# Performance work log

Measured on AMD Instinct MI355X. Metric: run time of the kernel, lower is better.

The kernel has to match this reference:

```python
import jax, jax.numpy as jnp
import numpy as np

B, H, W, C = 4, 112, 112, 256
WS, E, HEADS = 7, 3, 8
HD = C // HEADS                      # 32
WA = WS * WS                         # 49
NWIN = (H // WS) * (W // WS)         # 256
FOCAL_AREA = 49                      # focal_window^2
SCALE = HD ** -0.5

def _valid_ind_rolled():
    tl = np.ones((WS, WS)); tl[:-E, :-E] = 0
    tr = np.ones((WS, WS)); tr[:-E, E:] = 0
    bl = np.ones((WS, WS)); bl[E:, :-E] = 0
    br = np.ones((WS, WS)); br[E:, E:] = 0
    msk = np.stack([tl, tr, bl, br], 0).reshape(-1)
    return np.nonzero(msk == 1)[0]

VALID_IND = jnp.asarray(_valid_ind_rolled())   # (132,)
L_ROLL = WA + int(VALID_IND.shape[0])          # 181 = window_size_of_key

def window_partition(t):
    b = t.shape[0]
    t = t.reshape(b, H // WS, WS, W // WS, WS, C)
    return t.transpose(0, 1, 3, 2, 4, 5).reshape(-1, WA, C)

def split_heads(t):  # (n, L, C) -> (n, HEADS, L, HD)
    n, L, _ = t.shape
    return t.reshape(n, L, HEADS, HD).transpose(0, 2, 1, 3)

def setup_inputs():
    key = jax.random.key(0)
    ks = jax.random.split(key, 9)
    p = lambda k, s: jax.random.normal(k, s, jnp.float32) * 0.02
    return {
        "x": jax.random.normal(ks[0], (B, H, W, C), jnp.float32),
        "x_expanded": jax.random.normal(ks[1], (B * NWIN, 4 * WA, C), jnp.float32),
        "x_pooled": jax.random.normal(ks[2], (B * NWIN, FOCAL_AREA, C), jnp.float32),
        "mask_pooled": jnp.zeros((1, NWIN, FOCAL_AREA), jnp.float32),
        "q_w": p(ks[3], (C, C)), "q_b": jnp.zeros((C,), jnp.float32),
        "k_w": p(ks[4], (C, C)), "k_b": jnp.zeros((C,), jnp.float32),
        "v_w": p(ks[5], (C, C)), "v_b": jnp.zeros((C,), jnp.float32),
        "proj_w": p(ks[6], (C, C)), "proj_b": jnp.zeros((C,), jnp.float32),
        "rpb": p(ks[7], (1, HEADS, WA, L_ROLL)),
        "rpb_pooled": p(ks[8], (HEADS, WA, FOCAL_AREA)),
    }

def reference(x, x_expanded, x_pooled, mask_pooled,
              q_w, q_b, k_w, k_b, v_w, v_b, proj_w, proj_b,
              rpb, rpb_pooled):
    lin = lambda t, w, b: t @ w.T + b
    # window-local q/k/v: (B*NWIN, HEADS, WA, HD)
    q = split_heads(window_partition(lin(x, q_w, q_b))) * SCALE
    k_win = split_heads(window_partition(lin(x, k_w, k_b)))
    v_win = split_heads(window_partition(lin(x, v_w, v_b)))
    # expanded (rolled) keys/values, gathered by static valid indices
    xe = x_expanded[:, VALID_IND]                       # (B*NWIN, 132, C)
    k_exp = split_heads(lin(xe, k_w, k_b))
    v_exp = split_heads(lin(xe, v_w, v_b))
    # focal-pooled keys/values
    k_pool = split_heads(lin(x_pooled, k_w, k_b))
    v_pool = split_heads(lin(x_pooled, v_w, v_b))

    k_all = jnp.concatenate([k_win, k_exp, k_pool], axis=2)  # (B*NWIN,h,N,hd)
    v_all = jnp.concatenate([v_win, v_exp, v_pool], axis=2)

    attn = jnp.einsum("whqd,whkd->whqk", q, k_all)            # (B*NWIN,h,WA,N)
    attn = attn.at[:, :, :, :L_ROLL].add(rpb)
    mask_b = jnp.broadcast_to(
        mask_pooled[:, :, None, None, :], (B, NWIN, 1, 1, FOCAL_AREA)
    ).reshape(-1, 1, 1, FOCAL_AREA)
    attn = attn.at[:, :, :, L_ROLL:].add(rpb_pooled[None] + mask_b)
    attn = jax.nn.softmax(attn, axis=-1)
    out = jnp.einsum("whqk,whkd->whqd", attn, v_all)          # (B*NWIN,h,WA,hd)
    out = out.transpose(0, 2, 1, 3).reshape(-1, WA, C)
    return lin(out, proj_w, proj_b)
```

## Files before the change

### kernel.cpp

```cpp
#include <hip/hip_runtime.h>

typedef __attribute__((ext_vector_type(8))) __bf16 bf16x8;
typedef __attribute__((ext_vector_type(4))) float f32x4;

#define SCALE_Q 0.17677669529663687f

__constant__ int VALID_IND_C[132] = {
  4,5,6, 11,12,13, 18,19,20, 25,26,27,
  28,29,30,31,32,33,34, 35,36,37,38,39,40,41, 42,43,44,45,46,47,48,
  49,50,51, 56,57,58, 63,64,65, 70,71,72,
  77,78,79,80,81,82,83, 84,85,86,87,88,89,90, 91,92,93,94,95,96,97,
  98,99,100,101,102,103,104, 105,106,107,108,109,110,111, 112,113,114,115,116,117,118,
  123,124,125, 130,131,132, 137,138,139, 144,145,146,
  147,148,149,150,151,152,153, 154,155,156,157,158,159,160, 161,162,163,164,165,166,167,
  168,169,170, 175,176,177, 182,183,184, 189,190,191
};

__device__ __forceinline__ unsigned short f2bf(float f) {
  unsigned int u = __float_as_uint(f);
  u += 0x7fffu + ((u >> 16) & 1u);
  return (unsigned short)(u >> 16);
}

__device__ __forceinline__ uint4 pack8(const float4 a, const float4 b) {
  uint4 r;
  r.x = (unsigned)f2bf(a.x) | ((unsigned)f2bf(a.y) << 16);
  r.y = (unsigned)f2bf(a.z) | ((unsigned)f2bf(a.w) << 16);
  r.z = (unsigned)f2bf(b.x) | ((unsigned)f2bf(b.y) << 16);
  r.w = (unsigned)f2bf(b.z) | ((unsigned)f2bf(b.w) << 16);
  return r;
}

__global__ void prep_weights(const float* __restrict__ qw, const float* __restrict__ kw,
                             const float* __restrict__ vw, const float* __restrict__ pw,
                             unsigned short* __restrict__ wp) {
  int gid = blockIdx.x * 256 + threadIdx.x;
  int wsel = gid >> 16;
  int d = gid & 65535;
  const float* W = wsel == 0 ? qw : wsel == 1 ? kw : wsel == 2 ? vw : pw;
  int e = d & 7, ln = (d >> 3) & 63, ks = (d >> 9) & 7, cf = d >> 12;
  int c = cf * 16 + (ln & 15);
  int k = ks * 32 + ((ln >> 4) << 3) + e;
  wp[gid] = f2bf(W[c * 256 + k]);
}

__global__ void prep_bias(const float* __restrict__ rpb, const float* __restrict__ rpbp,
                          float* __restrict__ biasp) {
  int idx = blockIdx.x * 256 + threadIdx.x;
  int q = idx & 63, key = (idx >> 6) & 255, h = idx >> 14;
  int qc = q < 49 ? q : 48;
  float v;
  if (key < 181)      v = rpb[(h * 49 + qc) * 181 + key];
  else if (key < 230) v = rpbp[(h * 49 + qc) * 49 + (key - 181)];
  else                v = -1e30f;
  biasp[idx] = v;
}

__device__ __forceinline__ const float* kv_src_row(int w, int l, const float* x,
                                                   const float* xe, const float* xp) {
  if (l >= 230) l = 229;
  if (l < 49) {
    int b = w >> 8, win = w & 255;
    int wy = win >> 4, wx = win & 15;
    int iy = l / 7, ix = l - iy * 7;
    return x + (((b * 112 + wy * 7 + iy) * 112) + wx * 7 + ix) * 256;
  } else if (l < 181) {
    return xe + (w * 196 + VALID_IND_C[l - 49]) * 256;
  } else {
    return xp + (w * 49 + (l - 181)) * 256;
  }
}

__device__ __forceinline__ void gemm_core(const char* smem, const unsigned short* Wp,
                                          int nfbase, int lane, f32x4 acc[4][4]) {
  int arow = lane & 15, ahi = lane >> 4;
#pragma unroll
  for (int ks = 0; ks < 8; ++ks) {
    bf16x8 a[4];
#pragma unroll
    for (int m = 0; m < 4; ++m)
      a[m] = *(const bf16x8*)(smem + (m * 16 + arow) * 528 + ks * 64 + ahi * 16);
#pragma unroll
    for (int n = 0; n < 4; ++n) {
      bf16x8 b = *(const bf16x8*)(Wp + (((nfbase + n) * 8 + ks) * 64 + lane) * 8);
#pragma unroll
      for (int m = 0; m < 4; ++m)
        acc[m][n] = __builtin_amdgcn_mfma_f32_16x16x32_bf16(a[m], b, acc[m][n], 0, 0, 0);
    }
  }
}

__global__ __launch_bounds__(512, 4) void kv_gemm(
    const float* __restrict__ x, const float* __restrict__ xe, const float* __restrict__ xp,
    const float* __restrict__ kb, const float* __restrict__ vb,
    const unsigned short* __restrict__ WpK, const unsigned short* __restrict__ WpV,
    unsigned short* __restrict__ Kg, unsigned short* __restrict__ Vtg) {
  __shared__ char smem[64 * 528];
  __shared__ char tbuf[256 * 144];
  int tid = threadIdx.x;
  int w = blockIdx.x >> 2, sub = blockIdx.x & 3;
  {
    int r = tid >> 3, seg = tid & 7;
    const float* src = kv_src_row(w, sub * 64 + r, x, xe, xp) + seg * 32;
    char* dst = smem + r * 528 + seg * 64;
#pragma unroll
    for (int i = 0; i < 4; ++i) {
      float4 a = ((const float4*)src)[i * 2];
      float4 b = ((const float4*)src)[i * 2 + 1];
      *(uint4*)(dst + i * 16) = pack8(a, b);
    }
  }
  __syncthreads();
  int lane = tid & 63, wv = tid >> 6;
  bool isV = wv >= 4;
  int colq = wv & 3;
  const unsigned short* Wp = isV ? WpV : WpK;
  f32x4 acc[4][4];
#pragma unroll
  for (int m = 0; m < 4; ++m)
#pragma unroll
    for (int n = 0; n < 4; ++n) acc[m][n] = (f32x4){0.f, 0.f, 0.f, 0.f};
  gemm_core(smem, Wp, colq * 4, lane, acc);

  int arow = lane & 15, ahi = lane >> 4;
  const float* bias = isV ? vb : kb;
  __syncthreads();
  if (!isV) {
#pragma unroll
    for (int n = 0; n < 4; ++n) {
      int c = colq * 64 + n * 16 + arow;
      float bc = bias[c];
#pragma unroll
      for (int m = 0; m < 4; ++m)
#pragma unroll
        for (int reg = 0; reg < 4; ++reg)
          *(unsigned short*)(smem + (m * 16 + ahi * 4 + reg) * 528 + c * 2) =
              f2bf(acc[m][n][reg] + bc);
    }
  } else {
#pragma unroll
    for (int n = 0; n < 4; ++n) {
      int c = colq * 64 + n * 16 + arow;
      float bc = bias[c];
#pragma unroll
      for (int m = 0; m < 4; ++m)
#pragma unroll
        for (int reg = 0; reg < 4; ++reg)
          *(unsigned short*)(tbuf + c * 144 + (m * 16 + ahi * 4 + reg) * 2) =
              f2bf(acc[m][n][reg] + bc);
    }
  }
  __syncthreads();
  {
    int r = tid >> 3, seg = tid & 7;
    unsigned short* dst = Kg + (unsigned)(w * 256 + sub * 64 + r) * 256 + seg * 32;
    const char* s = smem + r * 528 + seg * 64;
#pragma unroll
    for (int i = 0; i < 4; ++i) *(uint4*)(dst + i * 8) = *(const uint4*)(s + i * 16);
  }
  {
    int c = tid >> 1, hf = tid & 1;
    unsigned short* dst = Vtg + (unsigned)(w * 256 + c) * 256 + sub * 64 + hf * 32;
    const char* s = tbuf + c * 144 + hf * 64;
#pragma unroll
    for (int i = 0; i < 4; ++i) *(uint4*)(dst + i * 8) = *(const uint4*)(s + i * 16);
  }
}

__global__ __launch_bounds__(256, 4) void q_gemm(
    const float* __restrict__ x, const float* __restrict__ qb,
    const unsigned short* __restrict__ WpQ, unsigned short* __restrict__ Qg) {
  __shared__ char smem[64 * 528];
  int tid = threadIdx.x;
  int w = blockIdx.x;
  int b = w >> 8, win = w & 255, wy = win >> 4, wx = win & 15;
  {
    int r = tid >> 2, seg = tid & 3;
    int rr = r < 49 ? r : 48;
    int iy = rr / 7, ix = rr - iy * 7;
    const float* src = x + (((b * 112 + wy * 7 + iy) * 112) + wx * 7 + ix) * 256 + seg * 64;
    char* dst = smem + r * 528 + seg * 128;
#pragma unroll
    for (int i = 0; i < 8; ++i) {
      float4 a = ((const float4*)src)[i * 2];
      float4 bb = ((const float4*)src)[i * 2 + 1];
      *(uint4*)(dst + i * 16) = pack8(a, bb);
    }
  }
  __syncthreads();
  int lane = tid & 63, wv = tid >> 6;
  f32x4 acc[4][4];
#pragma unroll
  for (int m = 0; m < 4; ++m)
#pragma unroll
    for (int n = 0; n < 4; ++n) acc[m][n] = (f32x4){0.f, 0.f, 0.f, 0.f};
  gemm_core(smem, WpQ, wv * 4, lane, acc);

  int arow = lane & 15, ahi = lane >> 4;
  __syncthreads();
#pragma unroll
  for (int n = 0; n < 4; ++n) {
    int c = wv * 64 + n * 16 + arow;
    float bc = qb[c];
#pragma unroll
    for (int m = 0; m < 4; ++m)
#pragma unroll
      for (int reg = 0; reg < 4; ++reg)
        *(unsigned short*)(smem + (m * 16 + ahi * 4 + reg) * 528 + c * 2) =
            f2bf((acc[m][n][reg] + bc) * SCALE_Q);
  }
  __syncthreads();
  {
    int r = tid >> 2, seg = tid & 3;
    unsigned short* dst = Qg + (unsigned)(w * 64 + r) * 256 + seg * 64;
    const char* s = smem + r * 528 + seg * 128;
#pragma unroll
    for (int i = 0; i < 8; ++i) *(uint4*)(dst + i * 8) = *(const uint4*)(s + i * 16);
  }
}

__global__ __launch_bounds__(512, 2) void attn_kernel(
    const unsigned short* __restrict__ Qg, const unsigned short* __restrict__ Kg,
    const unsigned short* __restrict__ Vtg, const float* __restrict__ biasp,
    const float* __restrict__ maskp, unsigned short* __restrict__ Og) {
  __shared__ char sK[64 * 528];
  __shared__ char sV[256 * 144];
  __shared__ char sP[8 * 64 * 144];
  int tid = threadIdx.x, lane = tid & 63, h = tid >> 6;
  int w = blockIdx.x, win = w & 255;
  int arow = lane & 15, ahi = lane >> 4;

  bf16x8 qa[4];
#pragma unroll
  for (int m = 0; m < 4; ++m)
    qa[m] = *(const bf16x8*)(Qg + (unsigned)(w * 64 + m * 16 + arow) * 256 + h * 32 + ahi * 8);

  f32x4 o[4][2];
  float mrun[4][4], lrun[4][4];
#pragma unroll
  for (int m = 0; m < 4; ++m) {
#pragma unroll
    for (int r = 0; r < 4; ++r) { mrun[m][r] = -1e30f; lrun[m][r] = 0.f; }
    o[m][0] = (f32x4){0.f, 0.f, 0.f, 0.f};
    o[m][1] = (f32x4){0.f, 0.f, 0.f, 0.f};
  }
  char* myP = sP + h * 9216;

  for (int t = 0; t < 4; ++t) {
    int kb = t * 64;
    __syncthreads();
    {
      int r = tid >> 3, seg = tid & 7;
      const unsigned short* src = Kg + (unsigned)(w * 256 + kb + r) * 256 + seg * 32;
      char* dst = sK + r * 528 + seg * 64;
#pragma unroll
      for (int i = 0; i < 4; ++i) *(uint4*)(dst + i * 16) = *(const uint4*)(src + i * 8);
      int c = tid >> 1, hf = tid & 1;
      const unsigned short* vs = Vtg + (unsigned)(w * 256 + c) * 256 + kb + hf * 32;
      char* vd = sV + c * 144 + hf * 64;
#pragma unroll
      for (int i = 0; i < 4; ++i) *(uint4*)(vd + i * 16) = *(const uint4*)(vs + i * 8);
    }
    __syncthreads();

    f32x4 s[4][4];
    {
      bf16x8 kf[4];
#pragma unroll
      for (int n = 0; n < 4; ++n)
        kf[n] = *(const bf16x8*)(sK + (n * 16 + arow) * 528 + h * 64 + ahi * 16);
#pragma unroll
      for (int m = 0; m < 4; ++m)
#pragma unroll
        for (int n = 0; n < 4; ++n)
          s[m][n] = __builtin_amdgcn_mfma_f32_16x16x32_bf16(qa[m], kf[n],
                      (f32x4){0.f, 0.f, 0.f, 0.f}, 0, 0, 0);
    }
#pragma unroll
    for (int n = 0; n < 4; ++n) {
      int key = kb + n * 16 + arow;
      float mk = 0.f;
      if (key >= 181 && key < 230) mk = maskp[win * 49 + (key - 181)];
      bool kvalid = key < 230;
#pragma unroll
      for (int m = 0; m < 4; ++m) {
        f32x4 bfr = *(const f32x4*)(biasp + (h * 256 + key) * 64 + m * 16 + ahi * 4);
#pragma unroll
        for (int reg = 0; reg < 4; ++reg)
          s[m][n][reg] = kvalid ? (s[m][n][reg] + bfr[reg] + mk) : -1e30f;
      }
    }
#pragma unroll
    for (int m = 0; m < 4; ++m) {
#pragma unroll
      for (int reg = 0; reg < 4; ++reg) {
        float mx = fmaxf(fmaxf(s[m][0][reg], s[m][1][reg]), fmaxf(s[m][2][reg], s[m][3][reg]));
#pragma unroll
        for (int d = 1; d < 16; d <<= 1) mx = fmaxf(mx, __shfl_xor(mx, d));
        float mold = mrun[m][reg];
        float mnew = fmaxf(mold, mx);
        float sc = __expf(mold - mnew);
        float rs = 0.f;
#pragma unroll
        for (int n = 0; n < 4; ++n) {
          float p = __expf(s[m][n][reg] - mnew);
          s[m][n][reg] = p;
          rs += p;
        }
#pragma unroll
        for (int d = 1; d < 16; d <<= 1) rs += __shfl_xor(rs, d);
        lrun[m][reg] = lrun[m][reg] * sc + rs;
        mrun[m][reg] = mnew;
        o[m][0][reg] *= sc;
        o[m][1][reg] *= sc;
      }
    }
#pragma unroll
    for (int m = 0; m < 4; ++m)
#pragma unroll
      for (int n = 0; n < 4; ++n) {
        char* base = myP + (m * 16 + ahi * 4) * 144 + (n * 16 + arow) * 2;
#pragma unroll
        for (int reg = 0; reg < 4; ++reg)
          *(unsigned short*)(base + reg * 144) = f2bf(s[m][n][reg]);
      }
    bf16x8 vf[2][2];
#pragma unroll
    for (int n2 = 0; n2 < 2; ++n2)
#pragma unroll
      for (int kv = 0; kv < 2; ++kv)
        vf[n2][kv] = *(const bf16x8*)(sV + (h * 32 + n2 * 16 + arow) * 144 + kv * 64 + ahi * 16);
#pragma unroll
    for (int m = 0; m < 4; ++m)
#pragma unroll
      for (int kv = 0; kv < 2; ++kv) {
        bf16x8 pf = *(const bf16x8*)(myP + (m * 16 + arow) * 144 + kv * 64 + ahi * 16);
#pragma unroll
        for (int n2 = 0; n2 < 2; ++n2)
          o[m][n2] = __builtin_amdgcn_mfma_f32_16x16x32_bf16(pf, vf[n2][kv], o[m][n2], 0, 0, 0);
      }
  }
  __syncthreads();
#pragma unroll
  for (int m = 0; m < 4; ++m)
#pragma unroll
    for (int n2 = 0; n2 < 2; ++n2)
#pragma unroll
      for (int reg = 0; reg < 4; ++reg) {
        int qrow = m * 16 + ahi * 4 + reg;
        float val = o[m][n2][reg] / lrun[m][reg];
        *(unsigned short*)(sK + qrow * 528 + (h * 32 + n2 * 16 + arow) * 2) = f2bf(val);
      }
  __syncthreads();
  for (int i = tid; i < 49 * 32; i += 512) {
    int r = i >> 5, seg = i & 31;
    *(uint4*)(Og + (unsigned)(w * 49 + r) * 256 + seg * 8) = *(const uint4*)(sK + r * 528 + seg * 16);
  }
}

__global__ __launch_bounds__(256, 4) void proj_gemm(
    const unsigned short* __restrict__ Og, const float* __restrict__ pb,
    const unsigned short* __restrict__ WpP, float* __restrict__ out) {
  __shared__ char smem[64 * 528];
  int tid = threadIdx.x;
  {
    int r = tid >> 2, seg = tid & 3;
    const unsigned short* src = Og + (unsigned)(blockIdx.x * 64 + r) * 256 + seg * 64;
    char* dst = smem + r * 528 + seg * 128;
#pragma unroll
    for (int i = 0; i < 8; ++i)
      *(uint4*)(dst + i * 16) = *(const uint4*)(src + i * 8);
  }
  __syncthreads();
  int lane = tid & 63, wv = tid >> 6;
  f32x4 acc[4][4];
#pragma unroll
  for (int m = 0; m < 4; ++m)
#pragma unroll
    for (int n = 0; n < 4; ++n) acc[m][n] = (f32x4){0.f, 0.f, 0.f, 0.f};
  gemm_core(smem, WpP, wv * 4, lane, acc);

  int arow = lane & 15, ahi = lane >> 4;
#pragma unroll
  for (int n = 0; n < 4; ++n) {
    int c = wv * 64 + n * 16 + arow;
    float bc = pb[c];
#pragma unroll
    for (int m = 0; m < 4; ++m) {
      int g = blockIdx.x * 64 + m * 16 + ahi * 4;
#pragma unroll
      for (int reg = 0; reg < 4; ++reg)
        out[(unsigned)(g + reg) * 256 + c] = acc[m][n][reg] + bc;
    }
  }
}

extern "C" void kernel_launch(void* const* d_in, const int* in_sizes, int n_in,
                              void* d_out, int out_size, void* d_ws, size_t ws_size,
                              hipStream_t stream) {
  (void)in_sizes; (void)n_in; (void)out_size;
  const float* x    = (const float*)d_in[0];
  const float* xe   = (const float*)d_in[1];
  const float* xp   = (const float*)d_in[2];
  const float* mask = (const float*)d_in[3];
  const float* qw   = (const float*)d_in[4];
  const float* qb   = (const float*)d_in[5];
  const float* kw   = (const float*)d_in[6];
  const float* kb   = (const float*)d_in[7];
  const float* vw   = (const float*)d_in[8];
  const float* vb   = (const float*)d_in[9];
  const float* pw   = (const float*)d_in[10];
  const float* pb   = (const float*)d_in[11];
  const float* rpb  = (const float*)d_in[12];
  const float* rpbp = (const float*)d_in[13];

  char* ws = (char*)d_ws;
  if (ws_size < 328728576ull) return;
  unsigned short* Wp  = (unsigned short*)(ws);
  float* biasp        = (float*)(ws + 524288);
  unsigned short* Qg  = (unsigned short*)(ws + 1048576);
  unsigned short* Kg  = (unsigned short*)(ws + 1048576 + 33554432);
  unsigned short* Vtg = (unsigned short*)(ws + 1048576 + 33554432 + 134217728);
  unsigned short* Og  = (unsigned short*)(ws + 1048576 + 33554432 + 2 * 134217728);
  const unsigned short* WpQ = Wp;
  const unsigned short* WpK = Wp + 65536;
  const unsigned short* WpV = Wp + 131072;
  const unsigned short* WpP = Wp + 196608;

  hipLaunchKernelGGL(prep_weights, dim3(1024), dim3(256), 0, stream, qw, kw, vw, pw, Wp);
  hipLaunchKernelGGL(prep_bias,    dim3(512),  dim3(256), 0, stream, rpb, rpbp, biasp);
  hipLaunchKernelGGL(q_gemm,       dim3(1024), dim3(256), 0, stream, x, qb, WpQ, Qg);
  hipLaunchKernelGGL(kv_gemm,      dim3(4096), dim3(512), 0, stream,
                     x, xe, xp, kb, vb, WpK, WpV, Kg, Vtg);
  hipLaunchKernelGGL(attn_kernel,  dim3(1024), dim3(512), 0, stream,
                     Qg, Kg, Vtg, biasp, mask, Og);
  hipLaunchKernelGGL(proj_gemm,    dim3(784),  dim3(256), 0, stream, Og, pb, WpP, (float*)d_out);
}
```

Measured before the change: 745.0 us.

## Keep attention probabilities in registers and drop online softmax in attn kernel

Attention now computes transposed score tiles so the bf16 probability fragment feeds the PV MFMA straight from registers, loading K/V fragments directly from global memory instead of staging them in LDS with per-tile barriers. The online max/rescale softmax is replaced with an unnormalized exp and a final row-sum division, and the bias table is transposed to match. kv_gemm reuses one LDS buffer and skips writing padded key rows, and attn occupancy bound is raised. Dropping max subtraction risks overflow for large scores, and unwritten padded K rows rely on the -inf bias.

```diff
diff --git a/kernel.cpp b/kernel.cpp
--- a/kernel.cpp
+++ b/kernel.cpp
@@ -47,7 +47,7 @@
 __global__ void prep_bias(const float* __restrict__ rpb, const float* __restrict__ rpbp,
                           float* __restrict__ biasp) {
   int idx = blockIdx.x * 256 + threadIdx.x;
-  int q = idx & 63, key = (idx >> 6) & 255, h = idx >> 14;
+  int key = idx & 255, q = (idx >> 8) & 63, h = idx >> 14;
   int qc = q < 49 ? q : 48;
   float v;
   if (key < 181)      v = rpb[(h * 49 + qc) * 181 + key];
@@ -95,8 +95,7 @@
     const float* __restrict__ kb, const float* __restrict__ vb,
     const unsigned short* __restrict__ WpK, const unsigned short* __restrict__ WpV,
     unsigned short* __restrict__ Kg, unsigned short* __restrict__ Vtg) {
-  __shared__ char smem[64 * 528];
-  __shared__ char tbuf[256 * 144];
+  __shared__ char smem[256 * 144];
   int tid = threadIdx.x;
   int w = blockIdx.x >> 2, sub = blockIdx.x & 3;
   {
@@ -137,7 +136,20 @@
           *(unsigned short*)(smem + (m * 16 + ahi * 4 + reg) * 528 + c * 2) =
               f2bf(acc[m][n][reg] + bc);
     }
-  } else {
+  }
+  __syncthreads();
+  {
+    int r = tid >> 3, seg = tid & 7;
+    int grow = sub * 64 + r;
+    if (grow < 230) {
+      unsigned short* dst = Kg + ((unsigned)w * 256 + grow) * 256 + seg * 32;
+      const char* s = smem + r * 528 + seg * 64;
+#pragma unroll
+      for (int i = 0; i < 4; ++i) *(uint4*)(dst + i * 8) = *(const uint4*)(s + i * 16);
+    }
+  }
+  __syncthreads();
+  if (isV) {
 #pragma unroll
     for (int n = 0; n < 4; ++n) {
       int c = colq * 64 + n * 16 + arow;
@@ -146,22 +158,15 @@
       for (int m = 0; m < 4; ++m)
 #pragma unroll
         for (int reg = 0; reg < 4; ++reg)
-          *(unsigned short*)(tbuf + c * 144 + (m * 16 + ahi * 4 + reg) * 2) =
+          *(unsigned short*)(smem + c * 144 + (m * 16 + ahi * 4 + reg) * 2) =
               f2bf(acc[m][n][reg] + bc);
     }
   }
   __syncthreads();
   {
-    int r = tid >> 3, seg = tid & 7;
-    unsigned short* dst = Kg + (unsigned)(w * 256 + sub * 64 + r) * 256 + seg * 32;
-    const char* s = smem + r * 528 + seg * 64;
-#pragma unroll
-    for (int i = 0; i < 4; ++i) *(uint4*)(dst + i * 8) = *(const uint4*)(s + i * 16);
-  }
-  {
     int c = tid >> 1, hf = tid & 1;
-    unsigned short* dst = Vtg + (unsigned)(w * 256 + c) * 256 + sub * 64 + hf * 32;
-    const char* s = tbuf + c * 144 + hf * 64;
+    unsigned short* dst = Vtg + ((unsigned)w * 256 + c) * 256 + sub * 64 + hf * 32;
+    const char* s = smem + c * 144 + hf * 64;
 #pragma unroll
     for (int i = 0; i < 4; ++i) *(uint4*)(dst + i * 8) = *(const uint4*)(s + i * 16);
   }
@@ -219,142 +224,104 @@
   }
 }
 
-__global__ __launch_bounds__(512, 2) void attn_kernel(
+__global__ __launch_bounds__(512, 4) void attn_kernel(
     const unsigned short* __restrict__ Qg, const unsigned short* __restrict__ Kg,
     const unsigned short* __restrict__ Vtg, const float* __restrict__ biasp,
     const float* __restrict__ maskp, unsigned short* __restrict__ Og) {
-  __shared__ char sK[64 * 528];
-  __shared__ char sV[256 * 144];
-  __shared__ char sP[8 * 64 * 144];
+  __shared__ char sOut[64 * 528];
+  __shared__ float smask[49];
   int tid = threadIdx.x, lane = tid & 63, h = tid >> 6;
   int w = blockIdx.x, win = w & 255;
-  int arow = lane & 15, ahi = lane >> 4;
+  int ql = lane & 15, a = lane >> 4, a4 = a * 4;
+  if (tid < 49) smask[tid] = maskp[win * 49 + tid];
+  __syncthreads();
 
   bf16x8 qa[4];
 #pragma unroll
   for (int m = 0; m < 4; ++m)
-    qa[m] = *(const bf16x8*)(Qg + (unsigned)(w * 64 + m * 16 + arow) * 256 + h * 32 + ahi * 8);
+    qa[m] = *(const bf16x8*)(Qg + ((unsigned)w * 64 + m * 16 + ql) * 256 + h * 32 + a * 8);
 
   f32x4 o[4][2];
-  float mrun[4][4], lrun[4][4];
+  float psum[4];
 #pragma unroll
   for (int m = 0; m < 4; ++m) {
-#pragma unroll
-    for (int r = 0; r < 4; ++r) { mrun[m][r] = -1e30f; lrun[m][r] = 0.f; }
     o[m][0] = (f32x4){0.f, 0.f, 0.f, 0.f};
     o[m][1] = (f32x4){0.f, 0.f, 0.f, 0.f};
-  }
-  char* myP = sP + h * 9216;
-
-  for (int t = 0; t < 4; ++t) {
-    int kb = t * 64;
-    __syncthreads();
-    {
-      int r = tid >> 3, seg = tid & 7;
-      const unsigned short* src = Kg + (unsigned)(w * 256 + kb + r) * 256 + seg * 32;
-      char* dst = sK + r * 528 + seg * 64;
-#pragma unroll
-      for (int i = 0; i < 4; ++i) *(uint4*)(dst + i * 16) = *(const uint4*)(src + i * 8);
-      int c = tid >> 1, hf = tid & 1;
-      const unsigned short* vs = Vtg + (unsigned)(w * 256 + c) * 256 + kb + hf * 32;
-      char* vd = sV + c * 144 + hf * 64;
-#pragma unroll
-      for (int i = 0; i < 4; ++i) *(uint4*)(vd + i * 16) = *(const uint4*)(vs + i * 8);
-    }
-    __syncthreads();
-
-    f32x4 s[4][4];
-    {
-      bf16x8 kf[4];
-#pragma unroll
-      for (int n = 0; n < 4; ++n)
-        kf[n] = *(const bf16x8*)(sK + (n * 16 + arow) * 528 + h * 64 + ahi * 16);
-#pragma unroll
-      for (int m = 0; m < 4; ++m)
-#pragma unroll
-        for (int n = 0; n < 4; ++n)
-          s[m][n] = __builtin_amdgcn_mfma_f32_16x16x32_bf16(qa[m], kf[n],
-                      (f32x4){0.f, 0.f, 0.f, 0.f}, 0, 0, 0);
-    }
-#pragma unroll
-    for (int n = 0; n < 4; ++n) {
-      int key = kb + n * 16 + arow;
-      float mk = 0.f;
-      if (key >= 181 && key < 230) mk = maskp[win * 49 + (key - 181)];
-      bool kvalid = key < 230;
-#pragma unroll
-      for (int m = 0; m < 4; ++m) {
-        f32x4 bfr = *(const f32x4*)(biasp + (h * 256 + key) * 64 + m * 16 + ahi * 4);
-#pragma unroll
-        for (int reg = 0; reg < 4; ++reg)
-          s[m][n][reg] = kvalid ? (s[m][n][reg] + bfr[reg] + mk) : -1e30f;
+    psum[m] = 0.f;
+  }
+
+  const unsigned short* Kb = Kg + (unsigned)w * 65536 + h * 32 + a * 8;
+  const unsigned short* Vb = Vtg + (unsigned)w * 65536;
+  const float* Bb = biasp + h * 16384;
+
+  for (int t = 0; t < 8; ++t) {
+    int kbase = t * 32;
+    bf16x8 kf[2];
+#pragma unroll
+    for (int kblk = 0; kblk < 2; ++kblk)
+      kf[kblk] = *(const bf16x8*)(Kb + (unsigned)(kbase + kblk * 16 + ql) * 256);
+    bf16x8 vf[2];
+#pragma unroll
+    for (int n2 = 0; n2 < 2; ++n2) {
+      const unsigned short* vp = Vb + (unsigned)(h * 32 + n2 * 16 + ql) * 256 + kbase + a4;
+      union { uint2 d[2]; bf16x8 v; } u;
+      u.d[0] = *(const uint2*)vp;
+      u.d[1] = *(const uint2*)(vp + 16);
+      vf[n2] = u.v;
+    }
+    float mk[2][4];
+#pragma unroll
+    for (int kblk = 0; kblk < 2; ++kblk)
+#pragma unroll
+      for (int reg = 0; reg < 4; ++reg) {
+        int key = kbase + kblk * 16 + a4 + reg;
+        mk[kblk][reg] = (key >= 181 && key < 230) ? smask[key - 181] : 0.f;
       }
-    }
 #pragma unroll
     for (int m = 0; m < 4; ++m) {
+      f32x4 s0 = __builtin_amdgcn_mfma_f32_16x16x32_bf16(kf[0], qa[m],
+                   (f32x4){0.f, 0.f, 0.f, 0.f}, 0, 0, 0);
+      f32x4 s1 = __builtin_amdgcn_mfma_f32_16x16x32_bf16(kf[1], qa[m],
+                   (f32x4){0.f, 0.f, 0.f, 0.f}, 0, 0, 0);
+      const float* brow = Bb + (unsigned)(m * 16 + ql) * 256 + kbase + a4;
+      f32x4 b0 = *(const f32x4*)(brow);
+      f32x4 b1 = *(const f32x4*)(brow + 16);
+      float p[8];
 #pragma unroll
       for (int reg = 0; reg < 4; ++reg) {
-        float mx = fmaxf(fmaxf(s[m][0][reg], s[m][1][reg]), fmaxf(s[m][2][reg], s[m][3][reg]));
-#pragma unroll
-        for (int d = 1; d < 16; d <<= 1) mx = fmaxf(mx, __shfl_xor(mx, d));
-        float mold = mrun[m][reg];
-        float mnew = fmaxf(mold, mx);
-        float sc = __expf(mold - mnew);
-        float rs = 0.f;
-#pragma unroll
-        for (int n = 0; n < 4; ++n) {
-          float p = __expf(s[m][n][reg] - mnew);
-          s[m][n][reg] = p;
-          rs += p;
-        }
-#pragma unroll
-        for (int d = 1; d < 16; d <<= 1) rs += __shfl_xor(rs, d);
-        lrun[m][reg] = lrun[m][reg] * sc + rs;
-        mrun[m][reg] = mnew;
-        o[m][0][reg] *= sc;
-        o[m][1][reg] *= sc;
+        p[reg]     = __expf(s0[reg] + b0[reg] + mk[0][reg]);
+        p[4 + reg] = __expf(s1[reg] + b1[reg] + mk[1][reg]);
+        psum[m] += p[reg] + p[4 + reg];
       }
-    }
-#pragma unroll
-    for (int m = 0; m < 4; ++m)
-#pragma unroll
-      for (int n = 0; n < 4; ++n) {
-        char* base = myP + (m * 16 + ahi * 4) * 144 + (n * 16 + arow) * 2;
-#pragma unroll
-        for (int reg = 0; reg < 4; ++reg)
-          *(unsigned short*)(base + reg * 144) = f2bf(s[m][n][reg]);
+      union { unsigned u[4]; bf16x8 v; } pf;
+      pf.u[0] = (unsigned)f2bf(p[0]) | ((unsigned)f2bf(p[1]) << 16);
+      pf.u[1] = (unsigned)f2bf(p[2]) | ((unsigned)f2bf(p[3]) << 16);
+      pf.u[2] = (unsigned)f2bf(p[4]) | ((unsigned)f2bf(p[5]) << 16);
+      pf.u[3] = (unsigned)f2bf(p[6]) | ((unsigned)f2bf(p[7]) << 16);
+#pragma unroll
+      for (int n2 = 0; n2 < 2; ++n2)
+        o[m][n2] = __builtin_amdgcn_mfma_f32_16x16x32_bf16(vf[n2], pf.v, o[m][n2], 0, 0, 0);
+    }
+  }
+#pragma unroll
+  for (int m = 0; m < 4; ++m) {
+    float v = psum[m];
+    v += __shfl_xor(v, 16);
+    v += __shfl_xor(v, 32);
+    float inv = 1.0f / v;
+#pragma unroll
+    for (int n2 = 0; n2 < 2; ++n2)
+#pragma unroll
+      for (int reg = 0; reg < 4; ++reg) {
+        int q = m * 16 + ql;
+        int c = h * 32 + n2 * 16 + a4 + reg;
+        *(unsigned short*)(sOut + q * 528 + c * 2) = f2bf(o[m][n2][reg] * inv);
       }
-    bf16x8 vf[2][2];
-#pragma unroll
-    for (int n2 = 0; n2 < 2; ++n2)
-#pragma unroll
-      for (int kv = 0; kv < 2; ++kv)
-        vf[n2][kv] = *(const bf16x8*)(sV + (h * 32 + n2 * 16 + arow) * 144 + kv * 64 + ahi * 16);
-#pragma unroll
-    for (int m = 0; m < 4; ++m)
-#pragma unroll
-      for (int kv = 0; kv < 2; ++kv) {
-        bf16x8 pf = *(const bf16x8*)(myP + (m * 16 + arow) * 144 + kv * 64 + ahi * 16);
-#pragma unroll
-        for (int n2 = 0; n2 < 2; ++n2)
-          o[m][n2] = __builtin_amdgcn_mfma_f32_16x16x32_bf16(pf, vf[n2][kv], o[m][n2], 0, 0, 0);
-      }
-  }
-  __syncthreads();
-#pragma unroll
-  for (int m = 0; m < 4; ++m)
-#pragma unroll
-    for (int n2 = 0; n2 < 2; ++n2)
-#pragma unroll
-      for (int reg = 0; reg < 4; ++reg) {
-        int qrow = m * 16 + ahi * 4 + reg;
-        float val = o[m][n2][reg] / lrun[m][reg];
-        *(unsigned short*)(sK + qrow * 528 + (h * 32 + n2 * 16 + arow) * 2) = f2bf(val);
-      }
+  }
   __syncthreads();
   for (int i = tid; i < 49 * 32; i += 512) {
     int r = i >> 5, seg = i & 31;
-    *(uint4*)(Og + (unsigned)(w * 49 + r) * 256 + seg * 8) = *(const uint4*)(sK + r * 528 + seg * 16);
+    *(uint4*)(Og + (unsigned)(w * 49 + r) * 256 + seg * 8) = *(const uint4*)(sOut + r * 528 + seg * 16);
   }
 }
 
```

After: 688.1 us. 1.08x faster.
